# Optimization experiments

Hardware: AMD Instinct MI355X
Metric: run time of the kernel (lower is better)

The kernel has to match this reference:

```python
import jax, jax.numpy as jnp
import numpy as np

GRID_SIZE = 8
SPLINE_ORDER = 3
LAYERS = [256, 512, 512, 256]  # [input_dim] + hidden_dims
BATCH = 8192
BN_EPS = 1e-5


def make_grid(in_features):
    # efficient-kan/torchkan grid: uniform on [-1, 1] extended by spline_order on each side
    h = 2.0 / GRID_SIZE
    g = jnp.arange(-SPLINE_ORDER, GRID_SIZE + SPLINE_ORDER + 1, dtype=jnp.float32) * h - 1.0
    return jnp.broadcast_to(g, (in_features, g.shape[0]))  # (In, G + 2k + 1)


def b_splines(x, grid):
    # x: (B, In), grid: (In, G + 2k + 1) -> bases: (B, In, G + k)
    xg = x[:, :, None]
    bases = ((xg >= grid[:, :-1]) & (xg < grid[:, 1:])).astype(x.dtype)
    for k in range(1, SPLINE_ORDER + 1):
        left = (xg - grid[:, : -(k + 1)]) / (grid[:, k:-1] - grid[:, : -(k + 1)])
        right = (grid[:, k + 1 :] - xg) / (grid[:, k + 1 :] - grid[:, 1:-k])
        bases = left * bases[:, :, :-1] + right * bases[:, :, 1:]
    return bases


def kan_linear(x, grid, base_w, spline_w):
    # base path: GELU (exact, matching torch.nn.GELU) then linear
    base_out = jax.nn.gelu(x, approximate=False) @ base_w.T
    spline_out = jnp.einsum('bik,oik->bo', b_splines(x, grid), spline_w)
    return base_out + spline_out


def setup_inputs() -> dict:
    key = jax.random.key(0)
    ks = jax.random.split(key, 16)
    inp = {'x': jax.random.normal(ks[0], (BATCH, LAYERS[0]), dtype=jnp.float32)}
    n_bases = GRID_SIZE + SPLINE_ORDER
    for i, (fin, fout) in enumerate(zip(LAYERS[:-1], LAYERS[1:])):
        scale = 1.0 / np.sqrt(fin)
        inp[f'grid{i}'] = make_grid(fin)
        inp[f'base_w{i}'] = jax.random.normal(ks[1 + 3 * i], (fout, fin), dtype=jnp.float32) * scale
        inp[f'spline_w{i}'] = jax.random.normal(ks[2 + 3 * i], (fout, fin, n_bases), dtype=jnp.float32) * (0.1 * scale)
    d_out = LAYERS[-1]
    inp['bn_gamma'] = jnp.ones((d_out,), dtype=jnp.float32)
    inp['bn_beta'] = jnp.zeros((d_out,), dtype=jnp.float32)
    inp['bn_mean'] = jax.random.normal(ks[10], (d_out,), dtype=jnp.float32) * 0.1
    inp['bn_var'] = jax.random.uniform(ks[11], (d_out,), dtype=jnp.float32, minval=0.5, maxval=1.5)
    return inp


def reference(x, grid0, base_w0, spline_w0, grid1, base_w1, spline_w1, grid2, base_w2, spline_w2, bn_gamma, bn_beta, bn_mean, bn_var):
    h = kan_linear(x, grid0, base_w0, spline_w0)
    h = kan_linear(h, grid1, base_w1, spline_w1)
    h = kan_linear(h, grid2, base_w2, spline_w2)
    # BatchNorm1d in eval mode (running stats); Dropout is identity at inference
    return bn_gamma * (h - bn_mean) * jax.lax.rsqrt(bn_var + BN_EPS) + bn_beta
```

## Files before the change

kernel.cpp:

```cpp
#include <hip/hip_runtime.h>
#include <hip/hip_bf16.h>
#include <cstdint>


typedef unsigned short ushort_t;
typedef __bf16 bf16x8 __attribute__((ext_vector_type(8)));
typedef float f32x4 __attribute__((ext_vector_type(4)));
typedef _Float16 f16x4 __attribute__((ext_vector_type(4)));
typedef _Float16 f16x8 __attribute__((ext_vector_type(8)));

__device__ __forceinline__ ushort_t f2bf(float f) {
    __bf16 h = (__bf16)f;
    return __builtin_bit_cast(ushort_t, h);
}

__device__ __forceinline__ void gload_lds16(const void* g, void* lds) {
    __builtin_amdgcn_global_load_lds(
        (const __attribute__((address_space(1))) unsigned int*)(uintptr_t)g,
        (__attribute__((address_space(3))) unsigned int*)(unsigned int)(uintptr_t)lds,
        16, 0, 0);
}

__device__ __forceinline__ void expand12(float x, ushort_t* o) {
    float x3 = x * x * x;
    float y  = 0.7978845608028654f * (x + 0.044715f * x3);
    float e  = __expf(2.0f * y);
    float th = 1.0f - 2.0f / (e + 1.0f);
    o[0] = f2bf(0.5f * x * (1.0f + th));
    float xs = (x + 1.75f) * 4.0f;
#pragma unroll
    for (int j = 0; j < 11; ++j) {
        float t  = xs - (float)j;
        float a  = fabsf(t - 2.0f);
        float p1 = (3.0f * a - 6.0f) * a * a + 4.0f;
        float c  = 2.0f - a;
        float p2 = c * c * c;
        float v  = (a <= 1.0f) ? p1 : fmaxf(p2, 0.0f);
        o[1 + j] = f2bf(v * (1.0f / 6.0f));
    }
}

__device__ __forceinline__ void pack32(const ushort_t* s, uint4* o) {
#pragma unroll
    for (int c = 0; c < 4; ++c) {
        o[c].x = (unsigned)s[c * 8 + 0] | ((unsigned)s[c * 8 + 1] << 16);
        o[c].y = (unsigned)s[c * 8 + 2] | ((unsigned)s[c * 8 + 3] << 16);
        o[c].z = (unsigned)s[c * 8 + 4] | ((unsigned)s[c * 8 + 5] << 16);
        o[c].w = (unsigned)s[c * 8 + 6] | ((unsigned)s[c * 8 + 7] << 16);
    }
}

template <int KB, bool FROMX>
__global__ __launch_bounds__(256) void expand_tiled_kernel(
    const float* __restrict__ X, const _Float16* __restrict__ P,
    size_t pstride, ushort_t* __restrict__ A)
{
    constexpr int F = KB * 8 / 3;
    const int idx = blockIdx.x * 256 + threadIdx.x;
    const int b   = idx & 8191;
    const int cg  = idx >> 13;
    const int row = b & 255;
    const int p   = b >> 8;

    float h[32];
    if (FROMX) {
        const float4* xr = (const float4*)(X + (size_t)b * F + cg * 32);
#pragma unroll
        for (int v = 0; v < 8; ++v) {
            float4 f = xr[v];
            h[4 * v + 0] = f.x; h[4 * v + 1] = f.y;
            h[4 * v + 2] = f.z; h[4 * v + 3] = f.w;
        }
    } else {
#pragma unroll
        for (int u = 0; u < 32; ++u) h[u] = 0.f;
#pragma unroll
        for (int z = 0; z < 4; ++z) {
            const f16x8* pr = (const f16x8*)(P + z * pstride + (size_t)b * F + cg * 32);
#pragma unroll
            for (int v = 0; v < 4; ++v) {
                f16x8 a = pr[v];
#pragma unroll
                for (int e = 0; e < 8; ++e) h[8 * v + e] += (float)a[e];
            }
        }
    }

    const size_t lbase = ((size_t)p * KB + 12 * cg) * 256 + row;
#pragma unroll
    for (int ci8 = 0; ci8 < 4; ++ci8) {
        ushort_t us[96];
#pragma unroll
        for (int u = 0; u < 8; ++u) expand12(h[ci8 * 8 + u], us + 12 * u);
#pragma unroll
        for (int kk = 0; kk < 3; ++kk) {
            uint4 o[4];
            pack32(us + 32 * kk, o);
            uint4* dst = (uint4*)(A + (lbase + (size_t)(3 * ci8 + kk) * 256) * 32);
            dst[0] = o[0]; dst[1] = o[1]; dst[2] = o[2]; dst[3] = o[3];
        }
    }
}

__global__ __launch_bounds__(256) void pack_w_kernel(
    const float* __restrict__ bw, const float* __restrict__ sw,
    ushort_t* __restrict__ W, int total)
{
    int idx = blockIdx.x * 256 + threadIdx.x;
    if (idx >= total) return;
    union { ushort_t us[12]; uint2 v[3]; } pk;
    pk.us[0] = f2bf(bw[idx]);
    const float* s = sw + (size_t)idx * 11;
#pragma unroll
    for (int k = 0; k < 11; ++k) pk.us[1 + k] = f2bf(s[k]);
    uint2* dst = (uint2*)(W + (size_t)idx * 12);
    dst[0] = pk.v[0]; dst[1] = pk.v[1]; dst[2] = pk.v[2];
}

#define SLOTE 16384

__global__ __launch_bounds__(512, 2) void gemm_kernel(
    const ushort_t* __restrict__ A,
    const ushort_t* __restrict__ W,
    _Float16* __restrict__ C,
    int M, int N, int KBT, int scps)
{
    extern __shared__ __align__(16) ushort_t lds[];

    const int t   = threadIdx.x;
    const int l   = t & 63;
    const int w   = t >> 6;
    const int wm  = w >> 2;
    const int wn  = w & 3;
    const int l15 = l & 15;
    const int q   = l >> 4;
    const int K   = KBT << 5;
    const int blockN = blockIdx.y * 256;
    const int kb0 = blockIdx.z * scps;
    const int nt  = scps;
    _Float16* Cz = C + (size_t)blockIdx.z * M * N;

    const ushort_t* Apan = A + (size_t)blockIdx.x * KBT * 8192;
    const ushort_t* Wb   = W + (size_t)blockN * K;

    auto stage = [&](int kb, int slot) {
        ushort_t* da = lds + slot * SLOTE;
        ushort_t* db = da + 8192;
        const ushort_t* sa = Apan + (size_t)kb * 8192;
#pragma unroll
        for (int it = 0; it < 2; ++it) {
            int s = it * 512 + t;
            int row = s >> 2, g = (s & 3) ^ ((row >> 1) & 3);
            gload_lds16(sa + (row << 5) + (g << 3), da + s * 8);
        }
#pragma unroll
        for (int it = 0; it < 2; ++it) {
            int s = it * 512 + t;
            int row = s >> 2, g = (s & 3) ^ ((row >> 1) & 3);
            gload_lds16(Wb + ((size_t)row * K + (kb << 5) + (g << 3)), db + s * 8);
        }
    };

    auto ldfrags = [&](int slot, bf16x8* afr, bf16x8* bfr) {
        const ushort_t* Ac = lds + slot * SLOTE;
        const ushort_t* Bc = Ac + 8192;
#pragma unroll
        for (int ni = 0; ni < 4; ++ni) {
            int n = wn * 64 + ni * 16 + l15;
            bfr[ni] = *(const bf16x8*)&Bc[(size_t)((n << 2) + (q ^ ((n >> 1) & 3))) * 8];
        }
#pragma unroll
        for (int mi = 0; mi < 8; ++mi) {
            int m = wm * 128 + mi * 16 + l15;
            afr[mi] = *(const bf16x8*)&Ac[(size_t)((m << 2) + (q ^ ((m >> 1) & 3))) * 8];
        }
    };

    f32x4 acc[8][4];
#pragma unroll
    for (int i = 0; i < 8; ++i)
#pragma unroll
        for (int j = 0; j < 4; ++j) acc[i][j] = (f32x4){0.f, 0.f, 0.f, 0.f};

    stage(kb0 + 0, 0); stage(kb0 + 1, 1); stage(kb0 + 2, 2);
    asm volatile("s_waitcnt vmcnt(4)" ::: "memory");
    __builtin_amdgcn_s_barrier();

    bf16x8 aA[8], bA[4], aB[8], bB[4];
    ldfrags(0, aA, bA);
    asm volatile("s_waitcnt lgkmcnt(0)" ::: "memory");

    auto body = [&](int tt, bf16x8* ac, bf16x8* bc, bf16x8* an, bf16x8* bn) {
        if (tt + 3 < nt) stage(kb0 + tt + 3, (tt + 3) & 3);
        if (tt + 1 < nt) ldfrags((tt + 1) & 3, an, bn);
        __builtin_amdgcn_sched_barrier(0);
        __builtin_amdgcn_s_setprio(1);
#pragma unroll
        for (int mi = 0; mi < 8; ++mi)
#pragma unroll
            for (int ni = 0; ni < 4; ++ni)
                acc[mi][ni] = __builtin_amdgcn_mfma_f32_16x16x32_bf16(
                    ac[mi], bc[ni], acc[mi][ni], 0, 0, 0);
        __builtin_amdgcn_s_setprio(0);
        asm volatile("s_waitcnt lgkmcnt(0)" ::: "memory");
        if (tt + 3 < nt)      asm volatile("s_waitcnt vmcnt(4)" ::: "memory");
        else if (tt + 2 < nt) asm volatile("s_waitcnt vmcnt(0)" ::: "memory");
        __builtin_amdgcn_s_barrier();
    };

    for (int tt = 0; tt < nt; tt += 2) {
        body(tt,     aA, bA, aB, bB);
        body(tt + 1, aB, bB, aA, bA);
    }

    const int blockM = blockIdx.x * 256;
#pragma unroll
    for (int ni = 0; ni < 4; ++ni) {
        int n = blockN + wn * 64 + ni * 16 + l15;
#pragma unroll
        for (int mi = 0; mi < 8; ++mi) {
            int mb = blockM + wm * 128 + mi * 16 + q * 4;
#pragma unroll
            for (int r = 0; r < 4; ++r)
                Cz[(size_t)(mb + r) * N + n] = (_Float16)acc[mi][ni][r];
        }
    }
}

__global__ __launch_bounds__(256) void bn_reduce_kernel(
    const _Float16* __restrict__ Q, size_t qstride,
    const float* __restrict__ gamma, const float* __restrict__ beta,
    const float* __restrict__ mean,  const float* __restrict__ var,
    float4* __restrict__ out, int n4)
{
    int i = blockIdx.x * 256 + threadIdx.x;
    if (i >= n4) return;
    float sx = 0.f, sy = 0.f, sz = 0.f, sw = 0.f;
#pragma unroll
    for (int s = 0; s < 8; ++s) {
        f16x4 v = *(const f16x4*)(Q + s * qstride + 4 * (size_t)i);
        sx += (float)v.x; sy += (float)v.y; sz += (float)v.z; sw += (float)v.w;
    }
    int nb = (i * 4) & 255;
    float4 g  = *(const float4*)(gamma + nb);
    float4 be = *(const float4*)(beta + nb);
    float4 mn = *(const float4*)(mean + nb);
    float4 vr = *(const float4*)(var + nb);
    float4 o;
    o.x = g.x * rsqrtf(vr.x + 1e-5f) * (sx - mn.x) + be.x;
    o.y = g.y * rsqrtf(vr.y + 1e-5f) * (sy - mn.y) + be.y;
    o.z = g.z * rsqrtf(vr.z + 1e-5f) * (sz - mn.z) + be.z;
    o.w = g.w * rsqrtf(vr.w + 1e-5f) * (sw - mn.w) + be.w;
    out[i] = o;
}

extern "C" void kernel_launch(void* const* d_in, const int* in_sizes, int n_in,
                              void* d_out, int out_size, void* d_ws, size_t ws_size,
                              hipStream_t stream) {
    const float* x     = (const float*)d_in[0];
    const float* bw0   = (const float*)d_in[2];
    const float* sw0   = (const float*)d_in[3];
    const float* bw1   = (const float*)d_in[5];
    const float* sw1   = (const float*)d_in[6];
    const float* bw2   = (const float*)d_in[8];
    const float* sw2   = (const float*)d_in[9];
    const float* gamma = (const float*)d_in[10];
    const float* beta  = (const float*)d_in[11];
    const float* mean  = (const float*)d_in[12];
    const float* var   = (const float*)d_in[13];

    char* ws = (char*)d_ws;
    ushort_t*  Abuf = (ushort_t*)(ws);
    ushort_t*  W0   = (ushort_t*)(ws + 100663296);
    ushort_t*  W1   = (ushort_t*)(ws + 103809024);
    ushort_t*  W2   = (ushort_t*)(ws + 110100480);
    _Float16*  P    = (_Float16*)(ws + 113246208);
    float*     out  = (float*)d_out;

    const size_t PS01 = (size_t)8192 * 512;
    const size_t PS2  = (size_t)8192 * 256;
    const size_t GEMM_LDS = 4 * SLOTE * sizeof(ushort_t);

    pack_w_kernel<<<(512 * 256 + 255) / 256, 256, 0, stream>>>(bw0, sw0, W0, 512 * 256);
    pack_w_kernel<<<(512 * 512 + 255) / 256, 256, 0, stream>>>(bw1, sw1, W1, 512 * 512);
    pack_w_kernel<<<(256 * 512 + 255) / 256, 256, 0, stream>>>(bw2, sw2, W2, 256 * 512);

    expand_tiled_kernel<96, true><<<256, 256, 0, stream>>>(x, nullptr, 0, Abuf);
    {
        dim3 g(32, 2, 4);
        gemm_kernel<<<g, 512, GEMM_LDS, stream>>>(Abuf, W0, P, 8192, 512, 96, 24);
    }
    expand_tiled_kernel<192, false><<<512, 256, 0, stream>>>(nullptr, P, PS01, Abuf);
    {
        dim3 g(32, 2, 4);
        gemm_kernel<<<g, 512, GEMM_LDS, stream>>>(Abuf, W1, P, 8192, 512, 192, 48);
    }
    expand_tiled_kernel<192, false><<<512, 256, 0, stream>>>(nullptr, P, PS01, Abuf);
    {
        dim3 g(32, 1, 8);
        gemm_kernel<<<g, 512, GEMM_LDS, stream>>>(Abuf, W2, P, 8192, 256, 192, 24);
    }
    bn_reduce_kernel<<<2048, 256, 0, stream>>>(
        P, PS2, gamma, beta, mean, var, (float4*)out, 8192 * 256 / 4);
}
```

Baseline: 342.1 us.

## Fuse all layers into one cooperative persistent kernel with grid syncs

Replaces the sequence of pack, expand, GEMM and batchnorm launches with a single cooperative kernel of 256 blocks. Phases are separated by grid-wide barriers, and the block index is remapped inside each phase. The goal is to remove per-launch overhead and inter-kernel gaps. In exchange, every phase is pinned to 256 blocks of 512 threads, so the expand and BN phases lose parallelism, and grid.sync adds its own cost.

Result: slower. 643.4 us (+88.1%).

```diff
diff --git a/kernel.cpp b/kernel.cpp
--- a/kernel.cpp
+++ b/kernel.cpp
@@ -1,13 +1,20 @@
 #include <hip/hip_runtime.h>
+#include <hip/hip_cooperative_groups.h>
 #include <hip/hip_bf16.h>
 #include <cstdint>
 
+
+namespace cg = cooperative_groups;
 
 typedef unsigned short ushort_t;
 typedef __bf16 bf16x8 __attribute__((ext_vector_type(8)));
 typedef float f32x4 __attribute__((ext_vector_type(4)));
 typedef _Float16 f16x4 __attribute__((ext_vector_type(4)));
 typedef _Float16 f16x8 __attribute__((ext_vector_type(8)));
+
+#define SLOTE 16384
+#define PS01  ((size_t)8192 * 512)
+#define PS2   ((size_t)8192 * 256)
 
 __device__ __forceinline__ ushort_t f2bf(float f) {
     __bf16 h = (__bf16)f;
@@ -50,17 +57,32 @@
     }
 }
 
+__device__ __forceinline__ void pack_w_item(
+    const float* __restrict__ bw, const float* __restrict__ sw,
+    ushort_t* __restrict__ W, int idx)
+{
+    union { ushort_t us[12]; uint2 v[3]; } pk;
+    pk.us[0] = f2bf(bw[idx]);
+    const float* s = sw + (size_t)idx * 11;
+#pragma unroll
+    for (int k = 0; k < 11; ++k) pk.us[1 + k] = f2bf(s[k]);
+    uint2* dst = (uint2*)(W + (size_t)idx * 12);
+    dst[0] = pk.v[0]; dst[1] = pk.v[1]; dst[2] = pk.v[2];
+}
+
 template <int KB, bool FROMX>
-__global__ __launch_bounds__(256) void expand_tiled_kernel(
-    const float* __restrict__ X, const _Float16* __restrict__ P,
-    size_t pstride, ushort_t* __restrict__ A)
-{
-    constexpr int F = KB * 8 / 3;
-    const int idx = blockIdx.x * 256 + threadIdx.x;
-    const int b   = idx & 8191;
-    const int cg  = idx >> 13;
-    const int row = b & 255;
-    const int p   = b >> 8;
+__device__ __forceinline__ void expand_phase(
+    const float* __restrict__ X, const _Float16* __restrict__ Pp,
+    ushort_t* __restrict__ A, int bid, int t)
+{
+    constexpr int F   = KB * 8 / 3;
+    constexpr int NCG = F / 32;
+    const int p = bid & 31;
+    const int e = (bid >> 5) * 512 + t;
+    if (e >= 256 * NCG) return;
+    const int row = e & 255;
+    const int cg  = e >> 8;
+    const int b   = p * 256 + row;
 
     float h[32];
     if (FROMX) {
@@ -76,12 +98,12 @@
         for (int u = 0; u < 32; ++u) h[u] = 0.f;
 #pragma unroll
         for (int z = 0; z < 4; ++z) {
-            const f16x8* pr = (const f16x8*)(P + z * pstride + (size_t)b * F + cg * 32);
+            const f16x8* pr = (const f16x8*)(Pp + z * PS01 + (size_t)b * F + cg * 32);
 #pragma unroll
             for (int v = 0; v < 4; ++v) {
                 f16x8 a = pr[v];
 #pragma unroll
-                for (int e = 0; e < 8; ++e) h[8 * v + e] += (float)a[e];
+                for (int ee = 0; ee < 8; ++ee) h[8 * v + ee] += (float)a[ee];
             }
         }
     }
@@ -102,32 +124,15 @@
     }
 }
 
-__global__ __launch_bounds__(256) void pack_w_kernel(
-    const float* __restrict__ bw, const float* __restrict__ sw,
-    ushort_t* __restrict__ W, int total)
-{
-    int idx = blockIdx.x * 256 + threadIdx.x;
-    if (idx >= total) return;
-    union { ushort_t us[12]; uint2 v[3]; } pk;
-    pk.us[0] = f2bf(bw[idx]);
-    const float* s = sw + (size_t)idx * 11;
-#pragma unroll
-    for (int k = 0; k < 11; ++k) pk.us[1 + k] = f2bf(s[k]);
-    uint2* dst = (uint2*)(W + (size_t)idx * 12);
-    dst[0] = pk.v[0]; dst[1] = pk.v[1]; dst[2] = pk.v[2];
-}
-
-#define SLOTE 16384
-
-__global__ __launch_bounds__(512, 2) void gemm_kernel(
+__device__ void gemm_phase(
     const ushort_t* __restrict__ A,
     const ushort_t* __restrict__ W,
     _Float16* __restrict__ C,
-    int M, int N, int KBT, int scps)
+    int M, int N, int KBT, int scps,
+    int bx, int by, int bz, int t)
 {
     extern __shared__ __align__(16) ushort_t lds[];
 
-    const int t   = threadIdx.x;
     const int l   = t & 63;
     const int w   = t >> 6;
     const int wm  = w >> 2;
@@ -135,12 +140,12 @@
     const int l15 = l & 15;
     const int q   = l >> 4;
     const int K   = KBT << 5;
-    const int blockN = blockIdx.y * 256;
-    const int kb0 = blockIdx.z * scps;
+    const int blockN = by * 256;
+    const int kb0 = bz * scps;
     const int nt  = scps;
-    _Float16* Cz = C + (size_t)blockIdx.z * M * N;
-
-    const ushort_t* Apan = A + (size_t)blockIdx.x * KBT * 8192;
+    _Float16* Cz = C + (size_t)bz * M * N;
+
+    const ushort_t* Apan = A + (size_t)bx * KBT * 8192;
     const ushort_t* Wb   = W + (size_t)blockN * K;
 
     auto stage = [&](int kb, int slot) {
@@ -213,7 +218,7 @@
         body(tt + 1, aB, bB, aA, bA);
     }
 
-    const int blockM = blockIdx.x * 256;
+    const int blockM = bx * 256;
 #pragma unroll
     for (int ni = 0; ni < 4; ++ni) {
         int n = blockN + wn * 64 + ni * 16 + l15;
@@ -227,79 +232,102 @@
     }
 }
 
-__global__ __launch_bounds__(256) void bn_reduce_kernel(
-    const _Float16* __restrict__ Q, size_t qstride,
+__device__ __forceinline__ void bn_phase(
+    const _Float16* __restrict__ Q,
     const float* __restrict__ gamma, const float* __restrict__ beta,
     const float* __restrict__ mean,  const float* __restrict__ var,
-    float4* __restrict__ out, int n4)
-{
-    int i = blockIdx.x * 256 + threadIdx.x;
-    if (i >= n4) return;
-    float sx = 0.f, sy = 0.f, sz = 0.f, sw = 0.f;
-#pragma unroll
-    for (int s = 0; s < 8; ++s) {
-        f16x4 v = *(const f16x4*)(Q + s * qstride + 4 * (size_t)i);
-        sx += (float)v.x; sy += (float)v.y; sz += (float)v.z; sw += (float)v.w;
-    }
-    int nb = (i * 4) & 255;
-    float4 g  = *(const float4*)(gamma + nb);
-    float4 be = *(const float4*)(beta + nb);
-    float4 mn = *(const float4*)(mean + nb);
-    float4 vr = *(const float4*)(var + nb);
-    float4 o;
-    o.x = g.x * rsqrtf(vr.x + 1e-5f) * (sx - mn.x) + be.x;
-    o.y = g.y * rsqrtf(vr.y + 1e-5f) * (sy - mn.y) + be.y;
-    o.z = g.z * rsqrtf(vr.z + 1e-5f) * (sz - mn.z) + be.z;
-    o.w = g.w * rsqrtf(vr.w + 1e-5f) * (sw - mn.w) + be.w;
-    out[i] = o;
+    float4* __restrict__ out, int tid)
+{
+#pragma unroll
+    for (int k = 0; k < 4; ++k) {
+        int i = tid + k * 131072;
+        float sx = 0.f, sy = 0.f, sz = 0.f, sw = 0.f;
+#pragma unroll
+        for (int s = 0; s < 8; ++s) {
+            f16x4 v = *(const f16x4*)(Q + s * PS2 + 4 * (size_t)i);
+            sx += (float)v.x; sy += (float)v.y; sz += (float)v.z; sw += (float)v.w;
+        }
+        int nb = (i * 4) & 255;
+        float4 g  = *(const float4*)(gamma + nb);
+        float4 be = *(const float4*)(beta + nb);
+        float4 mn = *(const float4*)(mean + nb);
+        float4 vr = *(const float4*)(var + nb);
+        float4 o;
+        o.x = g.x * rsqrtf(vr.x + 1e-5f) * (sx - mn.x) + be.x;
+        o.y = g.y * rsqrtf(vr.y + 1e-5f) * (sy - mn.y) + be.y;
+        o.z = g.z * rsqrtf(vr.z + 1e-5f) * (sz - mn.z) + be.z;
+        o.w = g.w * rsqrtf(vr.w + 1e-5f) * (sw - mn.w) + be.w;
+        out[i] = o;
+    }
+}
+
+struct KArgs {
+    const float* x;
+    const float* bw0; const float* sw0;
+    const float* bw1; const float* sw1;
+    const float* bw2; const float* sw2;
+    const float* gamma; const float* beta;
+    const float* mean;  const float* var;
+    ushort_t* A; ushort_t* W0; ushort_t* W1; ushort_t* W2;
+    _Float16* P; float* out;
+};
+
+__global__ __launch_bounds__(512, 2) void fused_kernel(KArgs a)
+{
+    const int bid = blockIdx.x;
+    const int t   = threadIdx.x;
+    const int tid = bid * 512 + t;
+    cg::grid_group grid = cg::this_grid();
+
+    pack_w_item(a.bw0, a.sw0, a.W0, tid);
+    pack_w_item(a.bw1, a.sw1, a.W1, tid);
+    pack_w_item(a.bw1, a.sw1, a.W1, tid + 131072);
+    pack_w_item(a.bw2, a.sw2, a.W2, tid);
+    expand_phase<96, true>(a.x, nullptr, a.A, bid, t);
+    grid.sync();
+
+    gemm_phase(a.A, a.W0, a.P, 8192, 512, 96, 24, bid & 31, (bid >> 5) & 1, bid >> 6, t);
+    grid.sync();
+
+    expand_phase<192, false>(nullptr, a.P, a.A, bid, t);
+    grid.sync();
+
+    gemm_phase(a.A, a.W1, a.P, 8192, 512, 192, 48, bid & 31, (bid >> 5) & 1, bid >> 6, t);
+    grid.sync();
+
+    expand_phase<192, false>(nullptr, a.P, a.A, bid, t);
+    grid.sync();
+
+    gemm_phase(a.A, a.W2, a.P, 8192, 256, 192, 24, bid & 31, 0, bid >> 5, t);
+    grid.sync();
+
+    bn_phase(a.P, a.gamma, a.beta, a.mean, a.var, (float4*)a.out, tid);
 }
 
 extern "C" void kernel_launch(void* const* d_in, const int* in_sizes, int n_in,
                               void* d_out, int out_size, void* d_ws, size_t ws_size,
                               hipStream_t stream) {
-    const float* x     = (const float*)d_in[0];
-    const float* bw0   = (const float*)d_in[2];
-    const float* sw0   = (const float*)d_in[3];
-    const float* bw1   = (const float*)d_in[5];
-    const float* sw1   = (const float*)d_in[6];
-    const float* bw2   = (const float*)d_in[8];
-    const float* sw2   = (const float*)d_in[9];
-    const float* gamma = (const float*)d_in[10];
-    const float* beta  = (const float*)d_in[11];
-    const float* mean  = (const float*)d_in[12];
-    const float* var   = (const float*)d_in[13];
-
     char* ws = (char*)d_ws;
-    ushort_t*  Abuf = (ushort_t*)(ws);
-    ushort_t*  W0   = (ushort_t*)(ws + 100663296);
-    ushort_t*  W1   = (ushort_t*)(ws + 103809024);
-    ushort_t*  W2   = (ushort_t*)(ws + 110100480);
-    _Float16*  P    = (_Float16*)(ws + 113246208);
-    float*     out  = (float*)d_out;
-
-    const size_t PS01 = (size_t)8192 * 512;
-    const size_t PS2  = (size_t)8192 * 256;
-    const size_t GEMM_LDS = 4 * SLOTE * sizeof(ushort_t);
-
-    pack_w_kernel<<<(512 * 256 + 255) / 256, 256, 0, stream>>>(bw0, sw0, W0, 512 * 256);
-    pack_w_kernel<<<(512 * 512 + 255) / 256, 256, 0, stream>>>(bw1, sw1, W1, 512 * 512);
-    pack_w_kernel<<<(256 * 512 + 255) / 256, 256, 0, stream>>>(bw2, sw2, W2, 256 * 512);
-
-    expand_tiled_kernel<96, true><<<256, 256, 0, stream>>>(x, nullptr, 0, Abuf);
-    {
-        dim3 g(32, 2, 4);
-        gemm_kernel<<<g, 512, GEMM_LDS, stream>>>(Abuf, W0, P, 8192, 512, 96, 24);
-    }
-    expand_tiled_kernel<192, false><<<512, 256, 0, stream>>>(nullptr, P, PS01, Abuf);
-    {
-        dim3 g(32, 2, 4);
-        gemm_kernel<<<g, 512, GEMM_LDS, stream>>>(Abuf, W1, P, 8192, 512, 192, 48);
-    }
-    expand_tiled_kernel<192, false><<<512, 256, 0, stream>>>(nullptr, P, PS01, Abuf);
-    {
-        dim3 g(32, 1, 8);
-        gemm_kernel<<<g, 512, GEMM_LDS, stream>>>(Abuf, W2, P, 8192, 256, 192, 24);
-    }
-    bn_reduce_kernel<<<2048, 256, 0, stream>>>(
-        P, PS2, gamma, beta, mean, var, (float4*)out, 8192 * 256 / 4);
-}
+    KArgs args;
+    args.x     = (const float*)d_in[0];
+    args.bw0   = (const float*)d_in[2];
+    args.sw0   = (const float*)d_in[3];
+    args.bw1   = (const float*)d_in[5];
+    args.sw1   = (const float*)d_in[6];
+    args.bw2   = (const float*)d_in[8];
+    args.sw2   = (const float*)d_in[9];
+    args.gamma = (const float*)d_in[10];
+    args.beta  = (const float*)d_in[11];
+    args.mean  = (const float*)d_in[12];
+    args.var   = (const float*)d_in[13];
+    args.A     = (ushort_t*)(ws);
+    args.W0    = (ushort_t*)(ws + 100663296);
+    args.W1    = (ushort_t*)(ws + 103809024);
+    args.W2    = (ushort_t*)(ws + 110100480);
+    args.P     = (_Float16*)(ws + 113246208);
+    args.out   = (float*)d_out;
+
+    void* params[] = { (void*)&args };
+    hipLaunchCooperativeKernel((const void*)fused_kernel, dim3(256), dim3(512),
+                               params, 131072u, stream);
+}
```

## Load A fragments directly from global into registers and merge prep kernels

Applied to the files above, without the earlier changes.

The GEMM no longer stages the A tile through LDS. Each wave loads its A fragments straight from global memory into registers, relying on the pre-tiled layout, while only B is staged in LDS with a halved slot size and adjusted vmcnt waits. The three weight-packing launches and the first expansion are merged into a single prep kernel to cut launch overhead. Direct global A loads drop LDS traffic and halve LDS use, but they expose global latency to the MFMA loop and add register pressure.

New measurement: 389.2 us. 1.14x slower.

```diff
diff --git a/kernel.cpp b/kernel.cpp
--- a/kernel.cpp
+++ b/kernel.cpp
@@ -8,6 +8,9 @@
 typedef float f32x4 __attribute__((ext_vector_type(4)));
 typedef _Float16 f16x4 __attribute__((ext_vector_type(4)));
 typedef _Float16 f16x8 __attribute__((ext_vector_type(8)));
+
+#define PS01  ((size_t)8192 * 512)
+#define PS2   ((size_t)8192 * 256)
 
 __device__ __forceinline__ ushort_t f2bf(float f) {
     __bf16 h = (__bf16)f;
@@ -50,13 +53,25 @@
     }
 }
 
+__device__ __forceinline__ void pack_w_item(
+    const float* __restrict__ bw, const float* __restrict__ sw,
+    ushort_t* __restrict__ W, int idx)
+{
+    union { ushort_t us[12]; uint2 v[3]; } pk;
+    pk.us[0] = f2bf(bw[idx]);
+    const float* s = sw + (size_t)idx * 11;
+#pragma unroll
+    for (int k = 0; k < 11; ++k) pk.us[1 + k] = f2bf(s[k]);
+    uint2* dst = (uint2*)(W + (size_t)idx * 12);
+    dst[0] = pk.v[0]; dst[1] = pk.v[1]; dst[2] = pk.v[2];
+}
+
 template <int KB, bool FROMX>
-__global__ __launch_bounds__(256) void expand_tiled_kernel(
-    const float* __restrict__ X, const _Float16* __restrict__ P,
-    size_t pstride, ushort_t* __restrict__ A)
+__device__ __forceinline__ void expand_item(
+    const float* __restrict__ X, const _Float16* __restrict__ Pp,
+    ushort_t* __restrict__ A, int idx)
 {
     constexpr int F = KB * 8 / 3;
-    const int idx = blockIdx.x * 256 + threadIdx.x;
     const int b   = idx & 8191;
     const int cg  = idx >> 13;
     const int row = b & 255;
@@ -76,7 +91,7 @@
         for (int u = 0; u < 32; ++u) h[u] = 0.f;
 #pragma unroll
         for (int z = 0; z < 4; ++z) {
-            const f16x8* pr = (const f16x8*)(P + z * pstride + (size_t)b * F + cg * 32);
+            const f16x8* pr = (const f16x8*)(Pp + z * PS01 + (size_t)b * F + cg * 32);
 #pragma unroll
             for (int v = 0; v < 4; ++v) {
                 f16x8 a = pr[v];
@@ -102,22 +117,27 @@
     }
 }
 
-__global__ __launch_bounds__(256) void pack_w_kernel(
-    const float* __restrict__ bw, const float* __restrict__ sw,
-    ushort_t* __restrict__ W, int total)
-{
-    int idx = blockIdx.x * 256 + threadIdx.x;
-    if (idx >= total) return;
-    union { ushort_t us[12]; uint2 v[3]; } pk;
-    pk.us[0] = f2bf(bw[idx]);
-    const float* s = sw + (size_t)idx * 11;
-#pragma unroll
-    for (int k = 0; k < 11; ++k) pk.us[1 + k] = f2bf(s[k]);
-    uint2* dst = (uint2*)(W + (size_t)idx * 12);
-    dst[0] = pk.v[0]; dst[1] = pk.v[1]; dst[2] = pk.v[2];
-}
-
-#define SLOTE 16384
+__global__ __launch_bounds__(256) void prep_kernel(
+    const float* __restrict__ x,
+    const float* __restrict__ bw0, const float* __restrict__ sw0,
+    const float* __restrict__ bw1, const float* __restrict__ sw1,
+    const float* __restrict__ bw2, const float* __restrict__ sw2,
+    ushort_t* __restrict__ W0, ushort_t* __restrict__ W1,
+    ushort_t* __restrict__ W2, ushort_t* __restrict__ A)
+{
+    const int bid = blockIdx.x;
+    const int idx = bid * 256 + threadIdx.x;
+    if (bid < 512)       pack_w_item(bw0, sw0, W0, idx);
+    else if (bid < 1536) pack_w_item(bw1, sw1, W1, idx - 131072);
+    else if (bid < 2048) pack_w_item(bw2, sw2, W2, idx - 393216);
+    else expand_item<96, true>(x, nullptr, A, idx - 524288);
+}
+
+__global__ __launch_bounds__(256) void expand_kernel(
+    const _Float16* __restrict__ P, ushort_t* __restrict__ A)
+{
+    expand_item<192, false>(nullptr, P, A, blockIdx.x * 256 + threadIdx.x);
+}
 
 __global__ __launch_bounds__(512, 2) void gemm_kernel(
     const ushort_t* __restrict__ A,
@@ -142,17 +162,10 @@
 
     const ushort_t* Apan = A + (size_t)blockIdx.x * KBT * 8192;
     const ushort_t* Wb   = W + (size_t)blockN * K;
-
-    auto stage = [&](int kb, int slot) {
-        ushort_t* da = lds + slot * SLOTE;
-        ushort_t* db = da + 8192;
-        const ushort_t* sa = Apan + (size_t)kb * 8192;
-#pragma unroll
-        for (int it = 0; it < 2; ++it) {
-            int s = it * 512 + t;
-            int row = s >> 2, g = (s & 3) ^ ((row >> 1) & 3);
-            gload_lds16(sa + (row << 5) + (g << 3), da + s * 8);
-        }
+    const int aoff = ((wm * 128 + l15) << 5) + (q << 3);
+
+    auto stage_b = [&](int kb, int slot) {
+        ushort_t* db = lds + slot * 8192;
 #pragma unroll
         for (int it = 0; it < 2; ++it) {
             int s = it * 512 + t;
@@ -160,21 +173,20 @@
             gload_lds16(Wb + ((size_t)row * K + (kb << 5) + (g << 3)), db + s * 8);
         }
     };
-
-    auto ldfrags = [&](int slot, bf16x8* afr, bf16x8* bfr) {
-        const ushort_t* Ac = lds + slot * SLOTE;
-        const ushort_t* Bc = Ac + 8192;
+    auto ldfrags_b = [&](int slot, bf16x8* bfr) {
+        const ushort_t* Bc = lds + slot * 8192;
 #pragma unroll
         for (int ni = 0; ni < 4; ++ni) {
             int n = wn * 64 + ni * 16 + l15;
             bfr[ni] = *(const bf16x8*)&Bc[(size_t)((n << 2) + (q ^ ((n >> 1) & 3))) * 8];
         }
-#pragma unroll
-        for (int mi = 0; mi < 8; ++mi) {
-            int m = wm * 128 + mi * 16 + l15;
-            afr[mi] = *(const bf16x8*)&Ac[(size_t)((m << 2) + (q ^ ((m >> 1) & 3))) * 8];
-        }
     };
+    auto load_a = [&](int kb, bf16x8* afr) {
+        const ushort_t* sa = Apan + (size_t)kb * 8192 + aoff;
+#pragma unroll
+        for (int mi = 0; mi < 8; ++mi)
+            afr[mi] = *(const bf16x8*)(sa + mi * 512);
+    };
 
     f32x4 acc[8][4];
 #pragma unroll
@@ -182,17 +194,18 @@
 #pragma unroll
         for (int j = 0; j < 4; ++j) acc[i][j] = (f32x4){0.f, 0.f, 0.f, 0.f};
 
-    stage(kb0 + 0, 0); stage(kb0 + 1, 1); stage(kb0 + 2, 2);
-    asm volatile("s_waitcnt vmcnt(4)" ::: "memory");
+    bf16x8 aA[8], bA[4], aB[8], bB[4];
+
+    load_a(kb0, aA);
+    stage_b(kb0 + 0, 0); stage_b(kb0 + 1, 1); stage_b(kb0 + 2, 2);
+    asm volatile("s_waitcnt vmcnt(2)" ::: "memory");
     __builtin_amdgcn_s_barrier();
-
-    bf16x8 aA[8], bA[4], aB[8], bB[4];
-    ldfrags(0, aA, bA);
+    ldfrags_b(0, bA);
     asm volatile("s_waitcnt lgkmcnt(0)" ::: "memory");
 
     auto body = [&](int tt, bf16x8* ac, bf16x8* bc, bf16x8* an, bf16x8* bn) {
-        if (tt + 3 < nt) stage(kb0 + tt + 3, (tt + 3) & 3);
-        if (tt + 1 < nt) ldfrags((tt + 1) & 3, an, bn);
+        if (tt + 1 < nt) { ldfrags_b((tt + 1) & 3, bn); load_a(kb0 + tt + 1, an); }
+        if (tt + 3 < nt) stage_b(kb0 + tt + 3, (tt + 3) & 3);
         __builtin_amdgcn_sched_barrier(0);
         __builtin_amdgcn_s_setprio(1);
 #pragma unroll
@@ -203,8 +216,8 @@
                     ac[mi], bc[ni], acc[mi][ni], 0, 0, 0);
         __builtin_amdgcn_s_setprio(0);
         asm volatile("s_waitcnt lgkmcnt(0)" ::: "memory");
-        if (tt + 3 < nt)      asm volatile("s_waitcnt vmcnt(4)" ::: "memory");
-        else if (tt + 2 < nt) asm volatile("s_waitcnt vmcnt(0)" ::: "memory");
+        if (tt + 3 < nt) asm volatile("s_waitcnt vmcnt(2)" ::: "memory");
+        else             asm volatile("s_waitcnt vmcnt(0)" ::: "memory");
         __builtin_amdgcn_s_barrier();
     };
 
@@ -228,7 +241,7 @@
 }
 
 __global__ __launch_bounds__(256) void bn_reduce_kernel(
-    const _Float16* __restrict__ Q, size_t qstride,
+    const _Float16* __restrict__ Q,
     const float* __restrict__ gamma, const float* __restrict__ beta,
     const float* __restrict__ mean,  const float* __restrict__ var,
     float4* __restrict__ out, int n4)
@@ -238,7 +251,7 @@
     float sx = 0.f, sy = 0.f, sz = 0.f, sw = 0.f;
 #pragma unroll
     for (int s = 0; s < 8; ++s) {
-        f16x4 v = *(const f16x4*)(Q + s * qstride + 4 * (size_t)i);
+        f16x4 v = *(const f16x4*)(Q + s * PS2 + 4 * (size_t)i);
         sx += (float)v.x; sy += (float)v.y; sz += (float)v.z; sw += (float)v.w;
     }
     int nb = (i * 4) & 255;
@@ -277,29 +290,24 @@
     _Float16*  P    = (_Float16*)(ws + 113246208);
     float*     out  = (float*)d_out;
 
-    const size_t PS01 = (size_t)8192 * 512;
-    const size_t PS2  = (size_t)8192 * 256;
-    const size_t GEMM_LDS = 4 * SLOTE * sizeof(ushort_t);
-
-    pack_w_kernel<<<(512 * 256 + 255) / 256, 256, 0, stream>>>(bw0, sw0, W0, 512 * 256);
-    pack_w_kernel<<<(512 * 512 + 255) / 256, 256, 0, stream>>>(bw1, sw1, W1, 512 * 512);
-    pack_w_kernel<<<(256 * 512 + 255) / 256, 256, 0, stream>>>(bw2, sw2, W2, 256 * 512);
-
-    expand_tiled_kernel<96, true><<<256, 256, 0, stream>>>(x, nullptr, 0, Abuf);
+    const size_t GEMM_LDS = 65536;
+
+    prep_kernel<<<2304, 256, 0, stream>>>(x, bw0, sw0, bw1, sw1, bw2, sw2,
+                                          W0, W1, W2, Abuf);
     {
         dim3 g(32, 2, 4);
         gemm_kernel<<<g, 512, GEMM_LDS, stream>>>(Abuf, W0, P, 8192, 512, 96, 24);
     }
-    expand_tiled_kernel<192, false><<<512, 256, 0, stream>>>(nullptr, P, PS01, Abuf);
+    expand_kernel<<<512, 256, 0, stream>>>(P, Abuf);
     {
         dim3 g(32, 2, 4);
         gemm_kernel<<<g, 512, GEMM_LDS, stream>>>(Abuf, W1, P, 8192, 512, 192, 48);
     }
-    expand_tiled_kernel<192, false><<<512, 256, 0, stream>>>(nullptr, P, PS01, Abuf);
+    expand_kernel<<<512, 256, 0, stream>>>(P, Abuf);
     {
         dim3 g(32, 1, 8);
         gemm_kernel<<<g, 512, GEMM_LDS, stream>>>(Abuf, W2, P, 8192, 256, 192, 24);
     }
     bn_reduce_kernel<<<2048, 256, 0, stream>>>(
-        P, PS2, gamma, beta, mean, var, (float4*)out, 8192 * 256 / 4);
-}
+        P, gamma, beta, mean, var, (float4*)out, 8192 * 256 / 4);
+}
```
